# Kernel tuning notes

Measured on AMD Instinct MI355X. Metric: run time of the kernel, lower is better.

The kernel has to match this reference:

```python
import jax, jax.numpy as jnp
import numpy as np

N = 50000   # nodes
E = 800000  # edges (avg degree 16)
D = 64      # feature dim (input_dim == hidden_dim == output_dim for num_layer=2)
BN_EPS = 1e-5


def setup_inputs() -> dict:
    key = jax.random.key(0)
    ks = jax.random.split(key, 8)
    def lin_w(k, fan_in, fan_out):
        return jax.random.normal(k, (fan_in, fan_out), jnp.float32) / np.sqrt(fan_in).astype(np.float32)
    inp = {
        "x": jax.random.normal(ks[0], (N, D), jnp.float32),
        "edge_index": jax.random.randint(ks[1], (2, E), 0, N),
    }
    ki = 2
    for l in range(2):
        for s in ("a", "b"):
            inp[f"w{l}{s}"] = lin_w(ks[ki], D, D)
            inp[f"b{l}{s}"] = jnp.zeros((D,), jnp.float32)
            inp[f"g{l}{s}"] = jnp.ones((D,), jnp.float32)   # BN gamma
            inp[f"be{l}{s}"] = jnp.zeros((D,), jnp.float32)  # BN beta
            ki += 1
    inp["lin_w"] = lin_w(ks[6], 2 * D, D)  # JK cat of 2 layers -> 2D, final lin -> D
    inp["lin_b"] = jnp.zeros((D,), jnp.float32)
    return inp


def _bn(h, g, b):
    # BatchNorm1d in training mode: batch statistics over the node axis
    m = h.mean(axis=0)
    v = h.var(axis=0)
    return (h - m) * jax.lax.rsqrt(v + BN_EPS) * g + b


def _gin(h, src, dst, w1, b1, g1, be1, w2, b2, g2, be2):
    # GINConv with eps=0: (1+eps)*x_i + sum_{j->i} x_j, then MLP(Lin-BN-ReLU-Lin-BN-ReLU)
    agg = jax.ops.segment_sum(h[src], dst, num_segments=N) + h
    h = jax.nn.relu(_bn(agg @ w1 + b1, g1, be1))
    return jax.nn.relu(_bn(h @ w2 + b2, g2, be2))


def reference(x, edge_index, w0a, b0a, g0a, be0a, w0b, b0b, g0b, be0b,
              w1a, b1a, g1a, be1a, w1b, b1b, g1b, be1b, lin_w, lin_b):
    src, dst = edge_index[0], edge_index[1]
    h1 = _gin(x, src, dst, w0a, b0a, g0a, be0a, w0b, b0b, g0b, be0b)
    h2 = _gin(h1, src, dst, w1a, b1a, g1a, be1a, w1b, b1b, g1b, be1b)
    # JumpingKnowledge 'cat' over the conv outputs (res[1:]), then final linear
    return jnp.concatenate([h1, h2], axis=1) @ lin_w + lin_b
```

## Files before the change

### kernel.cpp

```cpp
#include <hip/hip_runtime.h>
#include <hip/hip_bf16.h>

#define NN 50000
#define NE 800000
#define BN_EPS 1e-5f
#define CHUNK 4096
#define NCH 196
#define NBK 196

typedef __attribute__((ext_vector_type(4))) float f32x4;
typedef __attribute__((ext_vector_type(8))) short s16x8;
typedef __attribute__((ext_vector_type(4))) short s16x4;

__device__ __forceinline__ float bf2f(__hip_bfloat16 v) { return __bfloat162float(v); }
__device__ __forceinline__ float bs2f(short v) {
    unsigned u = ((unsigned)(unsigned short)v) << 16;
    return __builtin_bit_cast(float, u);
}
__device__ __forceinline__ short f2bs(float v) {
    __hip_bfloat16 b = __float2bfloat16(v);
    return __builtin_bit_cast(short, b);
}

__global__ void prep_k(const int* __restrict__ dst, int* __restrict__ part,
                       const float* __restrict__ x, __hip_bfloat16* __restrict__ Xb,
                       const float* __restrict__ w0a, const float* __restrict__ w0b,
                       const float* __restrict__ w1a, const float* __restrict__ w1b,
                       const float* __restrict__ lw,
                       short* __restrict__ Wt0a, short* __restrict__ Wt0b,
                       short* __restrict__ Wt1a, short* __restrict__ Wt1b,
                       short* __restrict__ Wtf) {
    int b = blockIdx.x, t = threadIdx.x;
    if (b < NCH) {
        __shared__ int c[256];
        c[t] = 0;
        __syncthreads();
        int base = b * CHUNK;
        int n = NE - base; if (n > CHUNK) n = CHUNK;
        for (int i = t; i < n; i += 256) atomicAdd(&c[dst[base + i] >> 8], 1);
        __syncthreads();
        part[b * 256 + t] = c[t];
    } else if (b < 196 + 3125) {
        int i = (b - 196) * 256 + t;
        if (i < NN * 16) {
            f32x4 v = *(const f32x4*)(x + (size_t)i * 4);
            s16x4 ov;
            #pragma unroll
            for (int j = 0; j < 4; j++) ov[j] = f2bs(v[j]);
            *(s16x4*)((short*)Xb + (size_t)i * 4) = ov;
        }
    } else {
        int wb = b - 3321;
        if (wb < 4) {
            const float* W = wb == 0 ? w0a : wb == 1 ? w0b : wb == 2 ? w1a : w1b;
            short* Wt = wb == 0 ? Wt0a : wb == 1 ? Wt0b : wb == 2 ? Wt1a : Wt1b;
            for (int e = t; e < 4096; e += 256) {
                int k = e >> 6, n = e & 63;
                Wt[n * 64 + k] = f2bs(W[e]);
            }
        } else {
            for (int e = t; e < 8192; e += 256) {
                int k = e >> 6, n = e & 63;
                Wtf[n * 128 + k] = f2bs(lw[e]);
            }
        }
    }
}

__global__ void bscan_k(const int* __restrict__ part, int* __restrict__ bbase,
                        int* __restrict__ bres, int* __restrict__ off,
                        float* __restrict__ sums) {
    __shared__ int s[256];
    int t = threadIdx.x;
    int v = 0;
    for (int c = 0; c < NCH; c++) v += part[c * 256 + t];
    s[t] = v;
    __syncthreads();
    for (int d = 1; d < 256; d <<= 1) {
        int u = (t >= d) ? s[t - d] : 0;
        __syncthreads();
        s[t] += u;
        __syncthreads();
    }
    int ex = s[t] - v;
    bbase[t] = ex;
    bres[t] = ex;
    if (t == 0) { bbase[256] = NE; off[NN] = NE; }
    sums[t] = 0.f; sums[256 + t] = 0.f;
}

__global__ void bscatter_k(const int* __restrict__ src, const int* __restrict__ dst,
                           int* __restrict__ bres, int* __restrict__ ebuf) {
    __shared__ int cnt[256], loff[256], lcur[256], gst[256], sc[256];
    __shared__ int packed[CHUNK];
    int t = threadIdx.x;
    cnt[t] = 0;
    __syncthreads();
    int base = blockIdx.x * CHUNK;
    int n = NE - base; if (n > CHUNK) n = CHUNK;
    for (int i = t; i < n; i += 256) atomicAdd(&cnt[dst[base + i] >> 8], 1);
    __syncthreads();
    sc[t] = cnt[t];
    __syncthreads();
    for (int d = 1; d < 256; d <<= 1) {
        int u = (t >= d) ? sc[t - d] : 0;
        __syncthreads();
        sc[t] += u;
        __syncthreads();
    }
    loff[t] = sc[t] - cnt[t];
    lcur[t] = loff[t];
    __syncthreads();
    for (int i = t; i < n; i += 256) {
        int d = dst[base + i];
        int b = d >> 8;
        int p = atomicAdd(&lcur[b], 1);
        packed[p] = src[base + i] | ((d & 255) << 16) | (b << 24);
    }
    __syncthreads();
    if (cnt[t]) gst[t] = atomicAdd(&bres[t], cnt[t]);
    __syncthreads();
    for (int i = t; i < n; i += 256) {
        int v = packed[i];
        int b = (v >> 24) & 255;
        ebuf[gst[b] + i - loff[b]] = v & 0xFFFFFF;
    }
}

__global__ void csr_k(const int* __restrict__ bbase, const int* __restrict__ ebuf,
                      int* __restrict__ off, int* __restrict__ adj) {
    __shared__ int cnt[256], loff[256], lcur[256], sc[256];
    int b = blockIdx.x, t = threadIdx.x;
    int s0 = bbase[b], s1 = bbase[b + 1];
    int n = s1 - s0;
    cnt[t] = 0;
    __syncthreads();
    for (int i = t; i < n; i += 256) atomicAdd(&cnt[(ebuf[s0 + i] >> 16) & 255], 1);
    __syncthreads();
    sc[t] = cnt[t];
    __syncthreads();
    for (int d = 1; d < 256; d <<= 1) {
        int u = (t >= d) ? sc[t - d] : 0;
        __syncthreads();
        sc[t] += u;
        __syncthreads();
    }
    loff[t] = sc[t] - cnt[t];
    lcur[t] = loff[t];
    int node = b * 256 + t;
    if (node < NN) off[node] = s0 + loff[t];
    __syncthreads();
    for (int i = t; i < n; i += 256) {
        int v = ebuf[s0 + i];
        int p = atomicAdd(&lcur[(v >> 16) & 255], 1);
        adj[s0 + p] = v & 0xFFFF;
    }
}

__global__ void ggemm_k(const __hip_bfloat16* __restrict__ X,
                        const int* __restrict__ off, const int* __restrict__ adj,
                        const short* __restrict__ Wt,
                        const float* __restrict__ bias,
                        float* __restrict__ T,
                        float* __restrict__ sums) {
    __shared__ float lsum[64], lssq[64];
    int t = threadIdx.x;
    if (t < 64) { lsum[t] = 0.f; lssq[t] = 0.f; }
    __syncthreads();
    int wv = t >> 6, L = t & 63;
    int m = L & 15, quad = L >> 4;
    int wrow = blockIdx.x * 64 + wv * 16;
    int node = wrow + m;
    if (node >= NN) node = NN - 1;
    const short* Xp = (const short*)X;

    const short* rp = Xp + (size_t)node * 64 + quad * 8;
    s16x8 sl = *(const s16x8*)rp;
    s16x8 shh = *(const s16x8*)(rp + 32);
    float aL[8], aH[8];
    #pragma unroll
    for (int j = 0; j < 8; j++) { aL[j] = bs2f(sl[j]); aH[j] = bs2f(shh[j]); }

    int s = off[node], e = off[node + 1];
    int p = s;
    for (; p + 8 <= e; p += 8) {
        int jx[8];
        #pragma unroll
        for (int q = 0; q < 8; q++) jx[q] = adj[p + q];
        s16x8 v[8], w[8];
        #pragma unroll
        for (int q = 0; q < 8; q++) {
            const short* r = Xp + (size_t)jx[q] * 64 + quad * 8;
            v[q] = *(const s16x8*)r;
            w[q] = *(const s16x8*)(r + 32);
        }
        #pragma unroll
        for (int j = 0; j < 8; j++) {
            float sv = ((bs2f(v[0][j]) + bs2f(v[1][j])) + (bs2f(v[2][j]) + bs2f(v[3][j])))
                     + ((bs2f(v[4][j]) + bs2f(v[5][j])) + (bs2f(v[6][j]) + bs2f(v[7][j])));
            float sw = ((bs2f(w[0][j]) + bs2f(w[1][j])) + (bs2f(w[2][j]) + bs2f(w[3][j])))
                     + ((bs2f(w[4][j]) + bs2f(w[5][j])) + (bs2f(w[6][j]) + bs2f(w[7][j])));
            aL[j] += sv;
            aH[j] += sw;
        }
    }
    if (p + 4 <= e) {
        int j0 = adj[p], j1 = adj[p + 1], j2 = adj[p + 2], j3 = adj[p + 3];
        const short* r0 = Xp + (size_t)j0 * 64 + quad * 8;
        const short* r1 = Xp + (size_t)j1 * 64 + quad * 8;
        const short* r2 = Xp + (size_t)j2 * 64 + quad * 8;
        const short* r3 = Xp + (size_t)j3 * 64 + quad * 8;
        s16x8 v0 = *(const s16x8*)r0, w0 = *(const s16x8*)(r0 + 32);
        s16x8 v1 = *(const s16x8*)r1, w1 = *(const s16x8*)(r1 + 32);
        s16x8 v2 = *(const s16x8*)r2, w2 = *(const s16x8*)(r2 + 32);
        s16x8 v3 = *(const s16x8*)r3, w3 = *(const s16x8*)(r3 + 32);
        #pragma unroll
        for (int j = 0; j < 8; j++) {
            aL[j] += (bs2f(v0[j]) + bs2f(v1[j])) + (bs2f(v2[j]) + bs2f(v3[j]));
            aH[j] += (bs2f(w0[j]) + bs2f(w1[j])) + (bs2f(w2[j]) + bs2f(w3[j]));
        }
        p += 4;
    }
    for (; p < e; p++) {
        int j0 = adj[p];
        const short* r0 = Xp + (size_t)j0 * 64 + quad * 8;
        s16x8 v0 = *(const s16x8*)r0, w0 = *(const s16x8*)(r0 + 32);
        #pragma unroll
        for (int j = 0; j < 8; j++) { aL[j] += bs2f(v0[j]); aH[j] += bs2f(w0[j]); }
    }

    s16x8 a0, a1;
    #pragma unroll
    for (int j = 0; j < 8; j++) { a0[j] = f2bs(aL[j]); a1[j] = f2bs(aH[j]); }

    f32x4 acc[4];
    #pragma unroll
    for (int nt = 0; nt < 4; nt++) {
        int n = nt * 16 + m;
        s16x8 b0 = *(const s16x8*)(Wt + n * 64 + quad * 8);
        s16x8 b1 = *(const s16x8*)(Wt + n * 64 + 32 + quad * 8);
        acc[nt] = (f32x4){0.f, 0.f, 0.f, 0.f};
        acc[nt] = __builtin_amdgcn_mfma_f32_16x16x32_bf16(a0, b0, acc[nt], 0, 0, 0);
        acc[nt] = __builtin_amdgcn_mfma_f32_16x16x32_bf16(a1, b1, acc[nt], 0, 0, 0);
    }
    #pragma unroll
    for (int nt = 0; nt < 4; nt++) {
        int col = nt * 16 + m;
        float bv = bias[col];
        float ps = 0.f, pq = 0.f;
        #pragma unroll
        for (int r = 0; r < 4; r++) {
            int orow = wrow + quad * 4 + r;
            if (orow < NN) {
                float v = acc[nt][r] + bv;
                T[(size_t)orow * 64 + col] = v;
                ps += v;
                pq += v * v;
            }
        }
        atomicAdd(&lsum[col], ps);
        atomicAdd(&lssq[col], pq);
    }
    __syncthreads();
    if (t < 64) {
        atomicAdd(&sums[t], lsum[t]);
        atomicAdd(&sums[64 + t], lssq[t]);
    }
}

__global__ void gemm_bn_k(const float* __restrict__ Tin,
                          const float* __restrict__ stats,
                          const float* __restrict__ g, const float* __restrict__ be,
                          const short* __restrict__ Wt,
                          const float* __restrict__ bias,
                          float* __restrict__ T,
                          float* __restrict__ sums) {
    __shared__ float sc[64], sh[64], lsum[64], lssq[64];
    int tid = threadIdx.x;
    if (tid < 64) {
        float mm = stats[tid] * (1.0f / NN);
        float var = stats[64 + tid] * (1.0f / NN) - mm * mm;
        if (var < 0.f) var = 0.f;
        float s = g[tid] * rsqrtf(var + BN_EPS);
        sc[tid] = s;
        sh[tid] = be[tid] - mm * s;
        lsum[tid] = 0.f; lssq[tid] = 0.f;
    }
    __syncthreads();
    int wv = tid >> 6, L = tid & 63;
    int m = L & 15, quad = L >> 4;
    int wrow = blockIdx.x * 64 + wv * 16;
    int arow = wrow + m;
    if (arow >= NN) arow = NN - 1;
    f32x4 t0 = *(const f32x4*)(Tin + (size_t)arow * 64 + quad * 8);
    f32x4 t1 = *(const f32x4*)(Tin + (size_t)arow * 64 + quad * 8 + 4);
    f32x4 t2 = *(const f32x4*)(Tin + (size_t)arow * 64 + 32 + quad * 8);
    f32x4 t3 = *(const f32x4*)(Tin + (size_t)arow * 64 + 32 + quad * 8 + 4);
    s16x8 a0, a1;
    #pragma unroll
    for (int j = 0; j < 4; j++) {
        int k0 = quad * 8 + j, k1 = quad * 8 + 4 + j;
        float u0 = t0[j] * sc[k0] + sh[k0]; a0[j]     = f2bs(u0 > 0.f ? u0 : 0.f);
        float u1 = t1[j] * sc[k1] + sh[k1]; a0[4 + j] = f2bs(u1 > 0.f ? u1 : 0.f);
        float u2 = t2[j] * sc[32 + k0] + sh[32 + k0]; a1[j]     = f2bs(u2 > 0.f ? u2 : 0.f);
        float u3 = t3[j] * sc[32 + k1] + sh[32 + k1]; a1[4 + j] = f2bs(u3 > 0.f ? u3 : 0.f);
    }
    f32x4 acc[4];
    #pragma unroll
    for (int nt = 0; nt < 4; nt++) {
        int n = nt * 16 + m;
        s16x8 b0 = *(const s16x8*)(Wt + n * 64 + quad * 8);
        s16x8 b1 = *(const s16x8*)(Wt + n * 64 + 32 + quad * 8);
        acc[nt] = (f32x4){0.f, 0.f, 0.f, 0.f};
        acc[nt] = __builtin_amdgcn_mfma_f32_16x16x32_bf16(a0, b0, acc[nt], 0, 0, 0);
        acc[nt] = __builtin_amdgcn_mfma_f32_16x16x32_bf16(a1, b1, acc[nt], 0, 0, 0);
    }
    #pragma unroll
    for (int nt = 0; nt < 4; nt++) {
        int col = nt * 16 + m;
        float bv = bias[col];
        float ps = 0.f, pq = 0.f;
        #pragma unroll
        for (int r = 0; r < 4; r++) {
            int orow = wrow + quad * 4 + r;
            if (orow < NN) {
                float v = acc[nt][r] + bv;
                T[(size_t)orow * 64 + col] = v;
                ps += v;
                pq += v * v;
            }
        }
        atomicAdd(&lsum[col], ps);
        atomicAdd(&lssq[col], pq);
    }
    __syncthreads();
    if (tid < 64) {
        atomicAdd(&sums[tid], lsum[tid]);
        atomicAdd(&sums[64 + tid], lssq[tid]);
    }
}

__global__ void bn_k(const float* __restrict__ T, const float* __restrict__ sums,
                     const float* __restrict__ g, const float* __restrict__ be,
                     __hip_bfloat16* __restrict__ Hb) {
    __shared__ float sc[64], sh[64];
    int tid = threadIdx.x;
    if (tid < 64) {
        float m = sums[tid] * (1.0f / NN);
        float var = sums[64 + tid] * (1.0f / NN) - m * m;
        if (var < 0.f) var = 0.f;
        float s = g[tid] * rsqrtf(var + BN_EPS);
        sc[tid] = s;
        sh[tid] = be[tid] - m * s;
    }
    __syncthreads();
    int i = blockIdx.x * 256 + tid;
    if (i < NN * 16) {
        int row = i >> 4, f = (i & 15) * 4;
        f32x4 v = *(const f32x4*)(T + (size_t)row * 64 + f);
        s16x4 ub;
        #pragma unroll
        for (int j = 0; j < 4; j++) {
            float w = v[j] * sc[f + j] + sh[f + j];
            ub[j] = f2bs(w > 0.f ? w : 0.f);
        }
        *(s16x4*)((short*)Hb + (size_t)row * 64 + f) = ub;
    }
}

__global__ void gemm_fin_k(const __hip_bfloat16* __restrict__ H1b,
                           const float* __restrict__ T2,
                           const float* __restrict__ stats,
                           const float* __restrict__ g, const float* __restrict__ be,
                           const short* __restrict__ Wtf,
                           const float* __restrict__ bias,
                           float* __restrict__ O) {
    __shared__ float sc[64], sh[64];
    int tid = threadIdx.x;
    if (tid < 64) {
        float mm = stats[tid] * (1.0f / NN);
        float var = stats[64 + tid] * (1.0f / NN) - mm * mm;
        if (var < 0.f) var = 0.f;
        float s = g[tid] * rsqrtf(var + BN_EPS);
        sc[tid] = s;
        sh[tid] = be[tid] - mm * s;
    }
    __syncthreads();
    int wv = tid >> 6, L = tid & 63;
    int m = L & 15, quad = L >> 4;
    int wrow = blockIdx.x * 64 + wv * 16;
    int arow = wrow + m;
    if (arow >= NN) arow = NN - 1;
    const short* Hp = (const short*)H1b;
    s16x8 a0 = *(const s16x8*)(Hp + (size_t)arow * 64 + quad * 8);
    s16x8 a1 = *(const s16x8*)(Hp + (size_t)arow * 64 + 32 + quad * 8);
    f32x4 t0 = *(const f32x4*)(T2 + (size_t)arow * 64 + quad * 8);
    f32x4 t1 = *(const f32x4*)(T2 + (size_t)arow * 64 + quad * 8 + 4);
    f32x4 t2 = *(const f32x4*)(T2 + (size_t)arow * 64 + 32 + quad * 8);
    f32x4 t3 = *(const f32x4*)(T2 + (size_t)arow * 64 + 32 + quad * 8 + 4);
    s16x8 a2, a3;
    #pragma unroll
    for (int j = 0; j < 4; j++) {
        int k0 = quad * 8 + j, k1 = quad * 8 + 4 + j;
        float u0 = t0[j] * sc[k0] + sh[k0]; a2[j]     = f2bs(u0 > 0.f ? u0 : 0.f);
        float u1 = t1[j] * sc[k1] + sh[k1]; a2[4 + j] = f2bs(u1 > 0.f ? u1 : 0.f);
        float u2 = t2[j] * sc[32 + k0] + sh[32 + k0]; a3[j]     = f2bs(u2 > 0.f ? u2 : 0.f);
        float u3 = t3[j] * sc[32 + k1] + sh[32 + k1]; a3[4 + j] = f2bs(u3 > 0.f ? u3 : 0.f);
    }
    f32x4 acc[4];
    #pragma unroll
    for (int nt = 0; nt < 4; nt++) {
        int n = nt * 16 + m;
        s16x8 b0 = *(const s16x8*)(Wtf + n * 128 + quad * 8);
        s16x8 b1 = *(const s16x8*)(Wtf + n * 128 + 32 + quad * 8);
        s16x8 b2 = *(const s16x8*)(Wtf + n * 128 + 64 + quad * 8);
        s16x8 b3 = *(const s16x8*)(Wtf + n * 128 + 96 + quad * 8);
        acc[nt] = (f32x4){0.f, 0.f, 0.f, 0.f};
        acc[nt] = __builtin_amdgcn_mfma_f32_16x16x32_bf16(a0, b0, acc[nt], 0, 0, 0);
        acc[nt] = __builtin_amdgcn_mfma_f32_16x16x32_bf16(a1, b1, acc[nt], 0, 0, 0);
        acc[nt] = __builtin_amdgcn_mfma_f32_16x16x32_bf16(a2, b2, acc[nt], 0, 0, 0);
        acc[nt] = __builtin_amdgcn_mfma_f32_16x16x32_bf16(a3, b3, acc[nt], 0, 0, 0);
    }
    #pragma unroll
    for (int nt = 0; nt < 4; nt++) {
        int col = nt * 16 + m;
        float bv = bias[col];
        #pragma unroll
        for (int r = 0; r < 4; r++) {
            int orow = wrow + quad * 4 + r;
            if (orow < NN) O[(size_t)orow * 64 + col] = acc[nt][r] + bv;
        }
    }
}

extern "C" void kernel_launch(void* const* d_in, const int* in_sizes, int n_in,
                              void* d_out, int out_size, void* d_ws, size_t ws_size,
                              hipStream_t stream) {
    const float* x   = (const float*)d_in[0];
    const int*   ei  = (const int*)d_in[1];
    const float* w0a = (const float*)d_in[2];
    const float* b0a = (const float*)d_in[3];
    const float* g0a = (const float*)d_in[4];
    const float* be0a= (const float*)d_in[5];
    const float* w0b = (const float*)d_in[6];
    const float* b0b = (const float*)d_in[7];
    const float* g0b = (const float*)d_in[8];
    const float* be0b= (const float*)d_in[9];
    const float* w1a = (const float*)d_in[10];
    const float* b1a = (const float*)d_in[11];
    const float* g1a = (const float*)d_in[12];
    const float* be1a= (const float*)d_in[13];
    const float* w1b = (const float*)d_in[14];
    const float* b1b = (const float*)d_in[15];
    const float* g1b = (const float*)d_in[16];
    const float* be1b= (const float*)d_in[17];
    const float* lw  = (const float*)d_in[18];
    const float* lb  = (const float*)d_in[19];
    float* out = (float*)d_out;
    (void)in_sizes; (void)n_in; (void)out_size; (void)ws_size;

    char* wsb = (char*)d_ws;
    size_t o = 0;
    auto alloc = [&](size_t bytes) -> char* {
        char* p = wsb + o;
        o += (bytes + 255) & ~(size_t)255;
        return p;
    };
    int* part = (int*)alloc(NCH * 256 * 4);
    float* sums = (float*)alloc(512 * 4);
    int* bbase = (int*)alloc(257 * 4);
    int* bres = (int*)alloc(256 * 4);
    int* off = (int*)alloc((NN + 1) * 4);
    int* adj = (int*)alloc(NE * 4);
    int* ebuf = (int*)alloc(NE * 4);
    __hip_bfloat16* Xb  = (__hip_bfloat16*)alloc((size_t)NN * 64 * 2);
    __hip_bfloat16* HCb = (__hip_bfloat16*)alloc((size_t)NN * 64 * 2);
    float* T  = (float*)alloc((size_t)NN * 64 * 4);
    float* T2 = (float*)alloc((size_t)NN * 64 * 4);
    short* Wt0a = (short*)alloc(4096 * 2);
    short* Wt0b = (short*)alloc(4096 * 2);
    short* Wt1a = (short*)alloc(4096 * 2);
    short* Wt1b = (short*)alloc(4096 * 2);
    short* Wtf  = (short*)alloc(8192 * 2);

    const int* src = ei;
    const int* dst = ei + NE;

    prep_k<<<3326, 256, 0, stream>>>(dst, part, x, Xb, w0a, w0b, w1a, w1b, lw,
                                     Wt0a, Wt0b, Wt1a, Wt1b, Wtf);
    bscan_k<<<1, 256, 0, stream>>>(part, bbase, bres, off, sums);
    bscatter_k<<<NCH, 256, 0, stream>>>(src, dst, bres, ebuf);
    csr_k<<<NBK, 256, 0, stream>>>(bbase, ebuf, off, adj);

    const int mgrid = (NN + 63) / 64;
    const int agrid = (NN * 16 + 255) / 256;

    ggemm_k<<<mgrid, 256, 0, stream>>>(Xb, off, adj, Wt0a, b0a, T, sums + 0);
    gemm_bn_k<<<mgrid, 256, 0, stream>>>(T, sums + 0, g0a, be0a, Wt0b, b0b, T2, sums + 128);
    bn_k<<<agrid, 256, 0, stream>>>(T2, sums + 128, g0b, be0b, HCb);

    ggemm_k<<<mgrid, 256, 0, stream>>>(HCb, off, adj, Wt1a, b1a, T, sums + 256);
    gemm_bn_k<<<mgrid, 256, 0, stream>>>(T, sums + 256, g1a, be1a, Wt1b, b1b, T2, sums + 384);

    gemm_fin_k<<<mgrid, 256, 0, stream>>>(HCb, T2, sums + 384, g1b, be1b, Wtf, lb, out);
}
```

Baseline: 319.5 us.

## Fuse all stages into one persistent kernel with software grid barriers

Replaces the ten separate kernel launches with a single persistent kernel of 768 blocks. Blocks loop over the former grids and synchronize between stages with atomic-counter grid barriers, reset by a memset before launch. The aim is to remove launch overhead and inter-kernel gaps. In exchange, every barrier waits on the slowest block, and correctness depends on all 768 blocks being co-resident (launch bounds of 4 blocks per CU).

```diff
diff --git a/kernel.cpp b/kernel.cpp
--- a/kernel.cpp
+++ b/kernel.cpp
@@ -7,12 +7,14 @@
 #define CHUNK 4096
 #define NCH 196
 #define NBK 196
+#define GRID 768
+#define NGRP 782
+#define NPREP 3326
 
 typedef __attribute__((ext_vector_type(4))) float f32x4;
 typedef __attribute__((ext_vector_type(8))) short s16x8;
 typedef __attribute__((ext_vector_type(4))) short s16x4;
 
-__device__ __forceinline__ float bf2f(__hip_bfloat16 v) { return __bfloat162float(v); }
 __device__ __forceinline__ float bs2f(short v) {
     unsigned u = ((unsigned)(unsigned short)v) << 16;
     return __builtin_bit_cast(float, u);
@@ -22,157 +24,46 @@
     return __builtin_bit_cast(short, b);
 }
 
-__global__ void prep_k(const int* __restrict__ dst, int* __restrict__ part,
-                       const float* __restrict__ x, __hip_bfloat16* __restrict__ Xb,
-                       const float* __restrict__ w0a, const float* __restrict__ w0b,
-                       const float* __restrict__ w1a, const float* __restrict__ w1b,
-                       const float* __restrict__ lw,
-                       short* __restrict__ Wt0a, short* __restrict__ Wt0b,
-                       short* __restrict__ Wt1a, short* __restrict__ Wt1b,
-                       short* __restrict__ Wtf) {
-    int b = blockIdx.x, t = threadIdx.x;
-    if (b < NCH) {
-        __shared__ int c[256];
-        c[t] = 0;
-        __syncthreads();
-        int base = b * CHUNK;
-        int n = NE - base; if (n > CHUNK) n = CHUNK;
-        for (int i = t; i < n; i += 256) atomicAdd(&c[dst[base + i] >> 8], 1);
-        __syncthreads();
-        part[b * 256 + t] = c[t];
-    } else if (b < 196 + 3125) {
-        int i = (b - 196) * 256 + t;
-        if (i < NN * 16) {
-            f32x4 v = *(const f32x4*)(x + (size_t)i * 4);
-            s16x4 ov;
-            #pragma unroll
-            for (int j = 0; j < 4; j++) ov[j] = f2bs(v[j]);
-            *(s16x4*)((short*)Xb + (size_t)i * 4) = ov;
-        }
-    } else {
-        int wb = b - 3321;
-        if (wb < 4) {
-            const float* W = wb == 0 ? w0a : wb == 1 ? w0b : wb == 2 ? w1a : w1b;
-            short* Wt = wb == 0 ? Wt0a : wb == 1 ? Wt0b : wb == 2 ? Wt1a : Wt1b;
-            for (int e = t; e < 4096; e += 256) {
-                int k = e >> 6, n = e & 63;
-                Wt[n * 64 + k] = f2bs(W[e]);
-            }
-        } else {
-            for (int e = t; e < 8192; e += 256) {
-                int k = e >> 6, n = e & 63;
-                Wtf[n * 128 + k] = f2bs(lw[e]);
-            }
-        }
-    }
-}
-
-__global__ void bscan_k(const int* __restrict__ part, int* __restrict__ bbase,
-                        int* __restrict__ bres, int* __restrict__ off,
-                        float* __restrict__ sums) {
-    __shared__ int s[256];
-    int t = threadIdx.x;
-    int v = 0;
-    for (int c = 0; c < NCH; c++) v += part[c * 256 + t];
-    s[t] = v;
-    __syncthreads();
-    for (int d = 1; d < 256; d <<= 1) {
-        int u = (t >= d) ? s[t - d] : 0;
-        __syncthreads();
-        s[t] += u;
-        __syncthreads();
-    }
-    int ex = s[t] - v;
-    bbase[t] = ex;
-    bres[t] = ex;
-    if (t == 0) { bbase[256] = NE; off[NN] = NE; }
-    sums[t] = 0.f; sums[256 + t] = 0.f;
-}
-
-__global__ void bscatter_k(const int* __restrict__ src, const int* __restrict__ dst,
-                           int* __restrict__ bres, int* __restrict__ ebuf) {
-    __shared__ int cnt[256], loff[256], lcur[256], gst[256], sc[256];
-    __shared__ int packed[CHUNK];
-    int t = threadIdx.x;
-    cnt[t] = 0;
-    __syncthreads();
-    int base = blockIdx.x * CHUNK;
-    int n = NE - base; if (n > CHUNK) n = CHUNK;
-    for (int i = t; i < n; i += 256) atomicAdd(&cnt[dst[base + i] >> 8], 1);
-    __syncthreads();
-    sc[t] = cnt[t];
-    __syncthreads();
-    for (int d = 1; d < 256; d <<= 1) {
-        int u = (t >= d) ? sc[t - d] : 0;
-        __syncthreads();
-        sc[t] += u;
-        __syncthreads();
-    }
-    loff[t] = sc[t] - cnt[t];
-    lcur[t] = loff[t];
-    __syncthreads();
-    for (int i = t; i < n; i += 256) {
-        int d = dst[base + i];
-        int b = d >> 8;
-        int p = atomicAdd(&lcur[b], 1);
-        packed[p] = src[base + i] | ((d & 255) << 16) | (b << 24);
-    }
-    __syncthreads();
-    if (cnt[t]) gst[t] = atomicAdd(&bres[t], cnt[t]);
-    __syncthreads();
-    for (int i = t; i < n; i += 256) {
-        int v = packed[i];
-        int b = (v >> 24) & 255;
-        ebuf[gst[b] + i - loff[b]] = v & 0xFFFFFF;
-    }
-}
-
-__global__ void csr_k(const int* __restrict__ bbase, const int* __restrict__ ebuf,
-                      int* __restrict__ off, int* __restrict__ adj) {
-    __shared__ int cnt[256], loff[256], lcur[256], sc[256];
-    int b = blockIdx.x, t = threadIdx.x;
-    int s0 = bbase[b], s1 = bbase[b + 1];
-    int n = s1 - s0;
-    cnt[t] = 0;
-    __syncthreads();
-    for (int i = t; i < n; i += 256) atomicAdd(&cnt[(ebuf[s0 + i] >> 16) & 255], 1);
-    __syncthreads();
-    sc[t] = cnt[t];
-    __syncthreads();
-    for (int d = 1; d < 256; d <<= 1) {
-        int u = (t >= d) ? sc[t - d] : 0;
-        __syncthreads();
-        sc[t] += u;
-        __syncthreads();
-    }
-    loff[t] = sc[t] - cnt[t];
-    lcur[t] = loff[t];
-    int node = b * 256 + t;
-    if (node < NN) off[node] = s0 + loff[t];
-    __syncthreads();
-    for (int i = t; i < n; i += 256) {
-        int v = ebuf[s0 + i];
-        int p = atomicAdd(&lcur[(v >> 16) & 255], 1);
-        adj[s0 + p] = v & 0xFFFF;
-    }
-}
-
-__global__ void ggemm_k(const __hip_bfloat16* __restrict__ X,
-                        const int* __restrict__ off, const int* __restrict__ adj,
-                        const short* __restrict__ Wt,
-                        const float* __restrict__ bias,
-                        float* __restrict__ T,
-                        float* __restrict__ sums) {
-    __shared__ float lsum[64], lssq[64];
+struct Params {
+    const int* src; const int* dst;
+    const float* x;
+    const float *w0a, *b0a, *g0a, *be0a, *w0b, *b0b, *g0b, *be0b;
+    const float *w1a, *b1a, *g1a, *be1a, *w1b, *b1b, *g1b, *be1b;
+    const float *lw, *lb;
+    float* out;
+    int* part; float* sums; int* bbase; int* bres; int* off; int* adj; int* ebuf;
+    short* Xb; short* HCb; float* T; float* T2;
+    short *Wt0a, *Wt0b, *Wt1a, *Wt1b, *Wtf;
+    unsigned* bar;
+};
+
+__device__ __forceinline__ void gbar(unsigned* bar, int idx) {
+    __syncthreads();
+    if (threadIdx.x == 0) {
+        __threadfence();
+        __hip_atomic_fetch_add(&bar[idx], 1u, __ATOMIC_RELEASE, __HIP_MEMORY_SCOPE_AGENT);
+        while (__hip_atomic_load(&bar[idx], __ATOMIC_RELAXED, __HIP_MEMORY_SCOPE_AGENT)
+               < (unsigned)GRID) {
+            __builtin_amdgcn_s_sleep(2);
+        }
+        __threadfence();
+    }
+    __syncthreads();
+}
+
+__device__ __forceinline__ void ggemm_phase(int blk, const short* Xp,
+        const int* __restrict__ off, const int* __restrict__ adj,
+        const short* __restrict__ Wt, const float* __restrict__ bias,
+        float* __restrict__ T, float* __restrict__ sums, float* smf) {
+    float* lsum = smf; float* lssq = smf + 64;
     int t = threadIdx.x;
     if (t < 64) { lsum[t] = 0.f; lssq[t] = 0.f; }
     __syncthreads();
     int wv = t >> 6, L = t & 63;
     int m = L & 15, quad = L >> 4;
-    int wrow = blockIdx.x * 64 + wv * 16;
+    int wrow = blk * 64 + wv * 16;
     int node = wrow + m;
     if (node >= NN) node = NN - 1;
-    const short* Xp = (const short*)X;
 
     const short* rp = Xp + (size_t)node * 64 + quad * 8;
     s16x8 sl = *(const s16x8*)rp;
@@ -268,14 +159,13 @@
     }
 }
 
-__global__ void gemm_bn_k(const float* __restrict__ Tin,
-                          const float* __restrict__ stats,
-                          const float* __restrict__ g, const float* __restrict__ be,
-                          const short* __restrict__ Wt,
-                          const float* __restrict__ bias,
-                          float* __restrict__ T,
-                          float* __restrict__ sums) {
-    __shared__ float sc[64], sh[64], lsum[64], lssq[64];
+__device__ __forceinline__ void gemmbn_phase(int blk, const float* __restrict__ Tin,
+        const float* __restrict__ stats,
+        const float* __restrict__ g, const float* __restrict__ be,
+        const short* __restrict__ Wt, const float* __restrict__ bias,
+        float* __restrict__ T, float* __restrict__ sums, float* smf) {
+    float* sc = smf; float* sh = smf + 64;
+    float* lsum = smf + 128; float* lssq = smf + 192;
     int tid = threadIdx.x;
     if (tid < 64) {
         float mm = stats[tid] * (1.0f / NN);
@@ -289,7 +179,7 @@
     __syncthreads();
     int wv = tid >> 6, L = tid & 63;
     int m = L & 15, quad = L >> 4;
-    int wrow = blockIdx.x * 64 + wv * 16;
+    int wrow = blk * 64 + wv * 16;
     int arow = wrow + m;
     if (arow >= NN) arow = NN - 1;
     f32x4 t0 = *(const f32x4*)(Tin + (size_t)arow * 64 + quad * 8);
@@ -340,10 +230,11 @@
     }
 }
 
-__global__ void bn_k(const float* __restrict__ T, const float* __restrict__ sums,
-                     const float* __restrict__ g, const float* __restrict__ be,
-                     __hip_bfloat16* __restrict__ Hb) {
-    __shared__ float sc[64], sh[64];
+__device__ __forceinline__ void bn_phase(const float* __restrict__ T,
+        const float* __restrict__ sums,
+        const float* __restrict__ g, const float* __restrict__ be,
+        short* __restrict__ Hb, float* smf) {
+    float* sc = smf; float* sh = smf + 64;
     int tid = threadIdx.x;
     if (tid < 64) {
         float m = sums[tid] * (1.0f / NN);
@@ -354,28 +245,28 @@
         sh[tid] = be[tid] - m * s;
     }
     __syncthreads();
-    int i = blockIdx.x * 256 + tid;
-    if (i < NN * 16) {
-        int row = i >> 4, f = (i & 15) * 4;
-        f32x4 v = *(const f32x4*)(T + (size_t)row * 64 + f);
-        s16x4 ub;
-        #pragma unroll
-        for (int j = 0; j < 4; j++) {
-            float w = v[j] * sc[f + j] + sh[f + j];
-            ub[j] = f2bs(w > 0.f ? w : 0.f);
-        }
-        *(s16x4*)((short*)Hb + (size_t)row * 64 + f) = ub;
-    }
-}
-
-__global__ void gemm_fin_k(const __hip_bfloat16* __restrict__ H1b,
-                           const float* __restrict__ T2,
-                           const float* __restrict__ stats,
-                           const float* __restrict__ g, const float* __restrict__ be,
-                           const short* __restrict__ Wtf,
-                           const float* __restrict__ bias,
-                           float* __restrict__ O) {
-    __shared__ float sc[64], sh[64];
+    for (int blk = blockIdx.x; blk < 3125; blk += GRID) {
+        int i = blk * 256 + tid;
+        if (i < NN * 16) {
+            int row = i >> 4, f = (i & 15) * 4;
+            f32x4 v = *(const f32x4*)(T + (size_t)row * 64 + f);
+            s16x4 ub;
+            #pragma unroll
+            for (int j = 0; j < 4; j++) {
+                float w = v[j] * sc[f + j] + sh[f + j];
+                ub[j] = f2bs(w > 0.f ? w : 0.f);
+            }
+            *(s16x4*)(Hb + (size_t)row * 64 + f) = ub;
+        }
+    }
+}
+
+__device__ __forceinline__ void fin_phase(int blk, const short* __restrict__ Hp,
+        const float* __restrict__ T2, const float* __restrict__ stats,
+        const float* __restrict__ g, const float* __restrict__ be,
+        const short* __restrict__ Wtf, const float* __restrict__ bias,
+        float* __restrict__ O, float* smf) {
+    float* sc = smf; float* sh = smf + 64;
     int tid = threadIdx.x;
     if (tid < 64) {
         float mm = stats[tid] * (1.0f / NN);
@@ -388,10 +279,9 @@
     __syncthreads();
     int wv = tid >> 6, L = tid & 63;
     int m = L & 15, quad = L >> 4;
-    int wrow = blockIdx.x * 64 + wv * 16;
+    int wrow = blk * 64 + wv * 16;
     int arow = wrow + m;
     if (arow >= NN) arow = NN - 1;
-    const short* Hp = (const short*)H1b;
     s16x8 a0 = *(const s16x8*)(Hp + (size_t)arow * 64 + quad * 8);
     s16x8 a1 = *(const s16x8*)(Hp + (size_t)arow * 64 + 32 + quad * 8);
     f32x4 t0 = *(const f32x4*)(T2 + (size_t)arow * 64 + quad * 8);
@@ -433,30 +323,164 @@
     }
 }
 
+__global__ __launch_bounds__(256, 4) void fused_all(Params P) {
+    __shared__ int smem[5376];
+    float* smf = (float*)smem;
+    int t = threadIdx.x;
+
+    for (int b = blockIdx.x; b < NPREP; b += GRID) {
+        if (b < NCH) {
+            int* c = smem;
+            c[t] = 0;
+            __syncthreads();
+            int base = b * CHUNK;
+            int n = NE - base; if (n > CHUNK) n = CHUNK;
+            for (int i = t; i < n; i += 256) atomicAdd(&c[P.dst[base + i] >> 8], 1);
+            __syncthreads();
+            P.part[b * 256 + t] = c[t];
+            __syncthreads();
+        } else if (b < 196 + 3125) {
+            int i = (b - 196) * 256 + t;
+            if (i < NN * 16) {
+                f32x4 v = *(const f32x4*)(P.x + (size_t)i * 4);
+                s16x4 ov;
+                #pragma unroll
+                for (int j = 0; j < 4; j++) ov[j] = f2bs(v[j]);
+                *(s16x4*)(P.Xb + (size_t)i * 4) = ov;
+            }
+        } else {
+            int wb = b - 3321;
+            if (wb < 4) {
+                const float* W = wb == 0 ? P.w0a : wb == 1 ? P.w0b : wb == 2 ? P.w1a : P.w1b;
+                short* Wt = wb == 0 ? P.Wt0a : wb == 1 ? P.Wt0b : wb == 2 ? P.Wt1a : P.Wt1b;
+                for (int e = t; e < 4096; e += 256) {
+                    int k = e >> 6, n = e & 63;
+                    Wt[n * 64 + k] = f2bs(W[e]);
+                }
+            } else {
+                for (int e = t; e < 8192; e += 256) {
+                    int k = e >> 6, n = e & 63;
+                    P.Wtf[n * 128 + k] = f2bs(P.lw[e]);
+                }
+            }
+        }
+    }
+    gbar(P.bar, 0);
+
+    if (blockIdx.x == 0) {
+        int* s = smem;
+        int v = 0;
+        for (int c = 0; c < NCH; c++) v += P.part[c * 256 + t];
+        s[t] = v;
+        __syncthreads();
+        for (int d = 1; d < 256; d <<= 1) {
+            int u = (t >= d) ? s[t - d] : 0;
+            __syncthreads();
+            s[t] += u;
+            __syncthreads();
+        }
+        int ex = s[t] - v;
+        P.bbase[t] = ex;
+        P.bres[t] = ex;
+        if (t == 0) { P.bbase[256] = NE; P.off[NN] = NE; }
+        P.sums[t] = 0.f; P.sums[256 + t] = 0.f;
+    }
+    gbar(P.bar, 1);
+
+    if (blockIdx.x < NCH) {
+        int* cnt = smem;        int* loff = smem + 256;
+        int* lcur = smem + 512; int* gst = smem + 768;
+        int* sc = smem + 1024;  int* packed = smem + 1280;
+        cnt[t] = 0;
+        __syncthreads();
+        int base = blockIdx.x * CHUNK;
+        int n = NE - base; if (n > CHUNK) n = CHUNK;
+        for (int i = t; i < n; i += 256) atomicAdd(&cnt[P.dst[base + i] >> 8], 1);
+        __syncthreads();
+        sc[t] = cnt[t];
+        __syncthreads();
+        for (int d = 1; d < 256; d <<= 1) {
+            int u = (t >= d) ? sc[t - d] : 0;
+            __syncthreads();
+            sc[t] += u;
+            __syncthreads();
+        }
+        loff[t] = sc[t] - cnt[t];
+        lcur[t] = loff[t];
+        __syncthreads();
+        for (int i = t; i < n; i += 256) {
+            int d = P.dst[base + i];
+            int bb = d >> 8;
+            int pp = atomicAdd(&lcur[bb], 1);
+            packed[pp] = P.src[base + i] | ((d & 255) << 16) | (bb << 24);
+        }
+        __syncthreads();
+        if (cnt[t]) gst[t] = atomicAdd(&P.bres[t], cnt[t]);
+        __syncthreads();
+        for (int i = t; i < n; i += 256) {
+            int v = packed[i];
+            int bb = (v >> 24) & 255;
+            P.ebuf[gst[bb] + i - loff[bb]] = v & 0xFFFFFF;
+        }
+    }
+    gbar(P.bar, 2);
+
+    if (blockIdx.x < NBK) {
+        int* cnt = smem;        int* loff = smem + 256;
+        int* lcur = smem + 512; int* sc = smem + 768;
+        int b = blockIdx.x;
+        int s0 = P.bbase[b], s1 = P.bbase[b + 1];
+        int n = s1 - s0;
+        cnt[t] = 0;
+        __syncthreads();
+        for (int i = t; i < n; i += 256) atomicAdd(&cnt[(P.ebuf[s0 + i] >> 16) & 255], 1);
+        __syncthreads();
+        sc[t] = cnt[t];
+        __syncthreads();
+        for (int d = 1; d < 256; d <<= 1) {
+            int u = (t >= d) ? sc[t - d] : 0;
+            __syncthreads();
+            sc[t] += u;
+            __syncthreads();
+        }
+        loff[t] = sc[t] - cnt[t];
+        lcur[t] = loff[t];
+        int node = b * 256 + t;
+        if (node < NN) P.off[node] = s0 + loff[t];
+        __syncthreads();
+        for (int i = t; i < n; i += 256) {
+            int v = P.ebuf[s0 + i];
+            int pp = atomicAdd(&lcur[(v >> 16) & 255], 1);
+            P.adj[s0 + pp] = v & 0xFFFF;
+        }
+    }
+    gbar(P.bar, 3);
+
+    for (int blk = blockIdx.x; blk < NGRP; blk += GRID)
+        ggemm_phase(blk, P.Xb, P.off, P.adj, P.Wt0a, P.b0a, P.T, P.sums + 0, smf);
+    gbar(P.bar, 4);
+    for (int blk = blockIdx.x; blk < NGRP; blk += GRID)
+        gemmbn_phase(blk, P.T, P.sums + 0, P.g0a, P.be0a, P.Wt0b, P.b0b, P.T2, P.sums + 128, smf);
+    gbar(P.bar, 5);
+    bn_phase(P.T2, P.sums + 128, P.g0b, P.be0b, P.HCb, smf);
+    gbar(P.bar, 6);
+
+    for (int blk = blockIdx.x; blk < NGRP; blk += GRID)
+        ggemm_phase(blk, P.HCb, P.off, P.adj, P.Wt1a, P.b1a, P.T, P.sums + 256, smf);
+    gbar(P.bar, 7);
+    for (int blk = blockIdx.x; blk < NGRP; blk += GRID)
+        gemmbn_phase(blk, P.T, P.sums + 256, P.g1a, P.be1a, P.Wt1b, P.b1b, P.T2, P.sums + 384, smf);
+    gbar(P.bar, 8);
+
+    for (int blk = blockIdx.x; blk < NGRP; blk += GRID)
+        fin_phase(blk, P.HCb, P.T2, P.sums + 384, P.g1b, P.be1b, P.Wtf, P.lb, P.out, smf);
+}
+
 extern "C" void kernel_launch(void* const* d_in, const int* in_sizes, int n_in,
                               void* d_out, int out_size, void* d_ws, size_t ws_size,
                               hipStream_t stream) {
     const float* x   = (const float*)d_in[0];
     const int*   ei  = (const int*)d_in[1];
-    const float* w0a = (const float*)d_in[2];
-    const float* b0a = (const float*)d_in[3];
-    const float* g0a = (const float*)d_in[4];
-    const float* be0a= (const float*)d_in[5];
-    const float* w0b = (const float*)d_in[6];
-    const float* b0b = (const float*)d_in[7];
-    const float* g0b = (const float*)d_in[8];
-    const float* be0b= (const float*)d_in[9];
-    const float* w1a = (const float*)d_in[10];
-    const float* b1a = (const float*)d_in[11];
-    const float* g1a = (const float*)d_in[12];
-    const float* be1a= (const float*)d_in[13];
-    const float* w1b = (const float*)d_in[14];
-    const float* b1b = (const float*)d_in[15];
-    const float* g1b = (const float*)d_in[16];
-    const float* be1b= (const float*)d_in[17];
-    const float* lw  = (const float*)d_in[18];
-    const float* lb  = (const float*)d_in[19];
-    float* out = (float*)d_out;
     (void)in_sizes; (void)n_in; (void)out_size; (void)ws_size;
 
     char* wsb = (char*)d_ws;
@@ -466,41 +490,39 @@
         o += (bytes + 255) & ~(size_t)255;
         return p;
     };
-    int* part = (int*)alloc(NCH * 256 * 4);
-    float* sums = (float*)alloc(512 * 4);
-    int* bbase = (int*)alloc(257 * 4);
-    int* bres = (int*)alloc(256 * 4);
-    int* off = (int*)alloc((NN + 1) * 4);
-    int* adj = (int*)alloc(NE * 4);
-    int* ebuf = (int*)alloc(NE * 4);
-    __hip_bfloat16* Xb  = (__hip_bfloat16*)alloc((size_t)NN * 64 * 2);
-    __hip_bfloat16* HCb = (__hip_bfloat16*)alloc((size_t)NN * 64 * 2);
-    float* T  = (float*)alloc((size_t)NN * 64 * 4);
-    float* T2 = (float*)alloc((size_t)NN * 64 * 4);
-    short* Wt0a = (short*)alloc(4096 * 2);
-    short* Wt0b = (short*)alloc(4096 * 2);
-    short* Wt1a = (short*)alloc(4096 * 2);
-    short* Wt1b = (short*)alloc(4096 * 2);
-    short* Wtf  = (short*)alloc(8192 * 2);
-
-    const int* src = ei;
-    const int* dst = ei + NE;
-
-    prep_k<<<3326, 256, 0, stream>>>(dst, part, x, Xb, w0a, w0b, w1a, w1b, lw,
-                                     Wt0a, Wt0b, Wt1a, Wt1b, Wtf);
-    bscan_k<<<1, 256, 0, stream>>>(part, bbase, bres, off, sums);
-    bscatter_k<<<NCH, 256, 0, stream>>>(src, dst, bres, ebuf);
-    csr_k<<<NBK, 256, 0, stream>>>(bbase, ebuf, off, adj);
-
-    const int mgrid = (NN + 63) / 64;
-    const int agrid = (NN * 16 + 255) / 256;
-
-    ggemm_k<<<mgrid, 256, 0, stream>>>(Xb, off, adj, Wt0a, b0a, T, sums + 0);
-    gemm_bn_k<<<mgrid, 256, 0, stream>>>(T, sums + 0, g0a, be0a, Wt0b, b0b, T2, sums + 128);
-    bn_k<<<agrid, 256, 0, stream>>>(T2, sums + 128, g0b, be0b, HCb);
-
-    ggemm_k<<<mgrid, 256, 0, stream>>>(HCb, off, adj, Wt1a, b1a, T, sums + 256);
-    gemm_bn_k<<<mgrid, 256, 0, stream>>>(T, sums + 256, g1a, be1a, Wt1b, b1b, T2, sums + 384);
-
-    gemm_fin_k<<<mgrid, 256, 0, stream>>>(HCb, T2, sums + 384, g1b, be1b, Wtf, lb, out);
-}
+    Params P;
+    P.part = (int*)alloc(NCH * 256 * 4);
+    P.sums = (float*)alloc(512 * 4);
+    P.bbase = (int*)alloc(257 * 4);
+    P.bres = (int*)alloc(256 * 4);
+    P.off = (int*)alloc((NN + 1) * 4);
+    P.adj = (int*)alloc(NE * 4);
+    P.ebuf = (int*)alloc(NE * 4);
+    P.Xb  = (short*)alloc((size_t)NN * 64 * 2);
+    P.HCb = (short*)alloc((size_t)NN * 64 * 2);
+    P.T  = (float*)alloc((size_t)NN * 64 * 4);
+    P.T2 = (float*)alloc((size_t)NN * 64 * 4);
+    P.Wt0a = (short*)alloc(4096 * 2);
+    P.Wt0b = (short*)alloc(4096 * 2);
+    P.Wt1a = (short*)alloc(4096 * 2);
+    P.Wt1b = (short*)alloc(4096 * 2);
+    P.Wtf  = (short*)alloc(8192 * 2);
+    P.bar  = (unsigned*)alloc(16 * 4);
+
+    P.src = ei;
+    P.dst = ei + NE;
+    P.x   = x;
+    P.w0a = (const float*)d_in[2];  P.b0a = (const float*)d_in[3];
+    P.g0a = (const float*)d_in[4];  P.be0a = (const float*)d_in[5];
+    P.w0b = (const float*)d_in[6];  P.b0b = (const float*)d_in[7];
+    P.g0b = (const float*)d_in[8];  P.be0b = (const float*)d_in[9];
+    P.w1a = (const float*)d_in[10]; P.b1a = (const float*)d_in[11];
+    P.g1a = (const float*)d_in[12]; P.be1a = (const float*)d_in[13];
+    P.w1b = (const float*)d_in[14]; P.b1b = (const float*)d_in[15];
+    P.g1b = (const float*)d_in[16]; P.be1b = (const float*)d_in[17];
+    P.lw  = (const float*)d_in[18]; P.lb  = (const float*)d_in[19];
+    P.out = (float*)d_out;
+
+    hipMemsetAsync(P.bar, 0, 16 * sizeof(unsigned), stream);
+    fused_all<<<GRID, 256, 0, stream>>>(P);
+}
```

New measurement: 1.015 ms. 3.18x slower.

## Sort nodes by degree within buckets to balance gather-GEMM wavefronts

Applied to the files above, without the earlier changes.

The CSR build kernel now also computes a per-256-node-bucket permutation that orders nodes by descending in-degree (capped at 63) using a shared-memory counting sort. The aggregation+GEMM kernel reads this permutation, so each 16-row MFMA tile processes nodes of similar degree and writes outputs to their permuted rows. The goal is to reduce lane divergence and tail imbalance in the neighbor-gather loop. In exchange, csr_k does extra work, ggemm_k makes an extra indirection load, and its output writes are scattered.

```diff
diff --git a/kernel.cpp b/kernel.cpp
--- a/kernel.cpp
+++ b/kernel.cpp
@@ -7,12 +7,13 @@
 #define CHUNK 4096
 #define NCH 196
 #define NBK 196
+#define NSLOT 50176
+#define GGRID 784
 
 typedef __attribute__((ext_vector_type(4))) float f32x4;
 typedef __attribute__((ext_vector_type(8))) short s16x8;
 typedef __attribute__((ext_vector_type(4))) short s16x4;
 
-__device__ __forceinline__ float bf2f(__hip_bfloat16 v) { return __bfloat162float(v); }
 __device__ __forceinline__ float bs2f(short v) {
     unsigned u = ((unsigned)(unsigned short)v) << 16;
     return __builtin_bit_cast(float, u);
@@ -128,9 +129,11 @@
 }
 
 __global__ void csr_k(const int* __restrict__ bbase, const int* __restrict__ ebuf,
-                      int* __restrict__ off, int* __restrict__ adj) {
+                      int* __restrict__ off, int* __restrict__ adj,
+                      int* __restrict__ perm) {
     __shared__ int cnt[256], loff[256], lcur[256], sc[256];
     int b = blockIdx.x, t = threadIdx.x;
+    perm[b * 256 + t] = -1;
     int s0 = bbase[b], s1 = bbase[b + 1];
     int n = s1 - s0;
     cnt[t] = 0;
@@ -155,10 +158,36 @@
         int p = atomicAdd(&lcur[(v >> 16) & 255], 1);
         adj[s0 + p] = v & 0xFFFF;
     }
+    __syncthreads();
+    int key = -1;
+    if (node < NN) {
+        int deg = cnt[t];
+        if (deg > 63) deg = 63;
+        key = 63 - deg;
+    }
+    if (t < 64) loff[t] = 0;
+    __syncthreads();
+    if (key >= 0) atomicAdd(&loff[key], 1);
+    __syncthreads();
+    if (t < 64) sc[t] = loff[t];
+    __syncthreads();
+    for (int d = 1; d < 64; d <<= 1) {
+        int u = (t >= d && t < 64) ? sc[t - d] : 0;
+        __syncthreads();
+        if (t < 64) sc[t] += u;
+        __syncthreads();
+    }
+    if (t < 64) lcur[t] = sc[t] - loff[t];
+    __syncthreads();
+    if (key >= 0) {
+        int r = atomicAdd(&lcur[key], 1);
+        perm[b * 256 + r] = node;
+    }
 }
 
 __global__ void ggemm_k(const __hip_bfloat16* __restrict__ X,
                         const int* __restrict__ off, const int* __restrict__ adj,
+                        const int* __restrict__ perm,
                         const short* __restrict__ Wt,
                         const float* __restrict__ bias,
                         float* __restrict__ T,
@@ -170,8 +199,8 @@
     int wv = t >> 6, L = t & 63;
     int m = L & 15, quad = L >> 4;
     int wrow = blockIdx.x * 64 + wv * 16;
-    int node = wrow + m;
-    if (node >= NN) node = NN - 1;
+    int pn = perm[wrow + m];
+    int node = pn < 0 ? NN - 1 : pn;
     const short* Xp = (const short*)X;
 
     const short* rp = Xp + (size_t)node * 64 + quad * 8;
@@ -182,6 +211,7 @@
     for (int j = 0; j < 8; j++) { aL[j] = bs2f(sl[j]); aH[j] = bs2f(shh[j]); }
 
     int s = off[node], e = off[node + 1];
+    if (pn < 0) e = s;
     int p = s;
     for (; p + 8 <= e; p += 8) {
         int jx[8];
@@ -243,6 +273,9 @@
         acc[nt] = __builtin_amdgcn_mfma_f32_16x16x32_bf16(a0, b0, acc[nt], 0, 0, 0);
         acc[nt] = __builtin_amdgcn_mfma_f32_16x16x32_bf16(a1, b1, acc[nt], 0, 0, 0);
     }
+    int onode[4];
+    #pragma unroll
+    for (int r = 0; r < 4; r++) onode[r] = perm[wrow + quad * 4 + r];
     #pragma unroll
     for (int nt = 0; nt < 4; nt++) {
         int col = nt * 16 + m;
@@ -250,10 +283,9 @@
         float ps = 0.f, pq = 0.f;
         #pragma unroll
         for (int r = 0; r < 4; r++) {
-            int orow = wrow + quad * 4 + r;
-            if (orow < NN) {
+            if (onode[r] >= 0) {
                 float v = acc[nt][r] + bv;
-                T[(size_t)orow * 64 + col] = v;
+                T[(size_t)onode[r] * 64 + col] = v;
                 ps += v;
                 pq += v * v;
             }
@@ -473,6 +505,7 @@
     int* off = (int*)alloc((NN + 1) * 4);
     int* adj = (int*)alloc(NE * 4);
     int* ebuf = (int*)alloc(NE * 4);
+    int* perm = (int*)alloc(NSLOT * 4);
     __hip_bfloat16* Xb  = (__hip_bfloat16*)alloc((size_t)NN * 64 * 2);
     __hip_bfloat16* HCb = (__hip_bfloat16*)alloc((size_t)NN * 64 * 2);
     float* T  = (float*)alloc((size_t)NN * 64 * 4);
@@ -490,17 +523,15 @@
                                      Wt0a, Wt0b, Wt1a, Wt1b, Wtf);
     bscan_k<<<1, 256, 0, stream>>>(part, bbase, bres, off, sums);
     bscatter_k<<<NCH, 256, 0, stream>>>(src, dst, bres, ebuf);
-    csr_k<<<NBK, 256, 0, stream>>>(bbase, ebuf, off, adj);
+    csr_k<<<NBK, 256, 0, stream>>>(bbase, ebuf, off, adj, perm);
 
     const int mgrid = (NN + 63) / 64;
     const int agrid = (NN * 16 + 255) / 256;
 
-    ggemm_k<<<mgrid, 256, 0, stream>>>(Xb, off, adj, Wt0a, b0a, T, sums + 0);
+    ggemm_k<<<GGRID, 256, 0, stream>>>(Xb, off, adj, perm, Wt0a, b0a, T, sums + 0);
     gemm_bn_k<<<mgrid, 256, 0, stream>>>(T, sums + 0, g0a, be0a, Wt0b, b0b, T2, sums + 128);
     bn_k<<<agrid, 256, 0, stream>>>(T2, sums + 128, g0b, be0b, HCb);
-
-    ggemm_k<<<mgrid, 256, 0, stream>>>(HCb, off, adj, Wt1a, b1a, T, sums + 256);
+    ggemm_k<<<GGRID, 256, 0, stream>>>(HCb, off, adj, perm, Wt1a, b1a, T, sums + 256);
     gemm_bn_k<<<mgrid, 256, 0, stream>>>(T, sums + 256, g1a, be1a, Wt1b, b1b, T2, sums + 384);
-
     gemm_fin_k<<<mgrid, 256, 0, stream>>>(HCb, T2, sums + 384, g1b, be1b, Wtf, lb, out);
 }
```

Measured after the change: 325.3 us. No clear change (+1.8%).
